# Kernel optimization log

Measured on AMD Instinct MI355X. Metric: run time of the kernel, lower is better.

The kernel has to match this reference:

```python
import jax, jax.numpy as jnp
import numpy as np

B, S, UNITS = 32, 2048, 512
D = 2 * UNITS  # 1024


def setup_inputs() -> dict:
    key = jax.random.key(0)
    ks = jax.random.split(key, 12)
    s = 1.0 / np.sqrt(D)
    mask = (jax.random.uniform(ks[0], (B, S)) < 0.9).astype(jnp.float32)
    mask = mask.at[:, 0].set(1.0)  # guarantee no all-zero row
    return {
        "dec_hidden": jax.random.normal(ks[1], (2, B, UNITS), dtype=jnp.float32),
        "enc_output": jax.random.normal(ks[2], (B, S, D), dtype=jnp.float32),
        "enc_pad_mask": mask,
        "prev_coverage": jax.random.uniform(ks[3], (B, S), dtype=jnp.float32) * 0.1,
        "Wh": jax.random.uniform(ks[4], (D, D), minval=-s, maxval=s),
        "bh": jax.random.uniform(ks[5], (D,), minval=-s, maxval=s),
        "Ws": jax.random.uniform(ks[6], (D, D), minval=-s, maxval=s),
        "bs": jax.random.uniform(ks[7], (D,), minval=-s, maxval=s),
        "Wc": jax.random.uniform(ks[8], (D, 1), minval=-1.0, maxval=1.0),
        "bc": jax.random.uniform(ks[9], (D,), minval=-1.0, maxval=1.0),
        "v": jax.random.uniform(ks[10], (1, D), minval=-s, maxval=s),
        "bv": jax.random.uniform(ks[11], (1,), minval=-s, maxval=s),
        "use_coverage": 1,
    }


def reference(dec_hidden, enc_output, enc_pad_mask, prev_coverage,
              Wh, bh, Ws, bs, Wc, bc, v, bv, use_coverage):
    # dec_hidden: (2, B, units) -> (B, 1, 2*units)
    dec = jnp.transpose(dec_hidden, (1, 0, 2)).reshape(dec_hidden.shape[1], 1, -1)
    enc_features = jnp.einsum('bsd,ed->bse', enc_output, Wh) + bh  # (B,S,D)
    dec_features = jnp.einsum('bod,ed->boe', dec, Ws) + bs          # (B,1,D)
    att_inputs = enc_features + dec_features
    if use_coverage:
        # Linear(1 -> D) applied to prev_coverage[..., None]
        coverage_features = prev_coverage[:, :, None] * Wc[:, 0][None, None, :] + bc
        att_inputs = att_inputs + coverage_features
    score = jnp.einsum('bsd,od->bso', jnp.tanh(att_inputs), v) + bv  # (B,S,1)
    attention_weights = jax.nn.softmax(score, axis=1)[..., 0]        # (B,S)
    attention_weights = attention_weights * enc_pad_mask
    attention_weights = attention_weights / jnp.sum(attention_weights, axis=1, keepdims=True)
    context_vector = jnp.einsum('bs,bsd->bd', attention_weights, enc_output)
    if use_coverage:
        coverage_vector = prev_coverage + attention_weights
        return context_vector, attention_weights, coverage_vector
    return context_vector, attention_weights
```

## Files before the change

### kernel.cpp

```cpp
#include <hip/hip_runtime.h>
#include <hip/hip_bf16.h>

#define BATCH 32
#define SEQ   2048
#define DIM   1024

typedef __attribute__((ext_vector_type(4))) float f32x4;
typedef __attribute__((ext_vector_type(8))) short short8;

static __device__ __forceinline__ ushort f2bf(float x) {
    __hip_bfloat16 h = __float2bfloat16(x);
    union { __hip_bfloat16 h; ushort u; } cv; cv.h = h;
    return cv.u;
}

__global__ __launch_bounds__(256) void kWhPack(const float* __restrict__ Wh,
                                               ushort* __restrict__ whbp) {
    int g = blockIdx.x * 256 + threadIdx.x;
    int l  = g & 63;
    int kb = (g >> 6) & 31;
    int eb = g >> 11;
    int e  = eb * 16 + (l & 15);
    int k0 = kb * 32 + (l >> 4) * 8;
    const float* src = Wh + (size_t)e * DIM + k0;
    float4 a = *(const float4*)src;
    float4 b = *(const float4*)(src + 4);
    union { ushort us[8]; uint4 u4; } pk;
    pk.us[0] = f2bf(a.x); pk.us[1] = f2bf(a.y); pk.us[2] = f2bf(a.z); pk.us[3] = f2bf(a.w);
    pk.us[4] = f2bf(b.x); pk.us[5] = f2bf(b.y); pk.us[6] = f2bf(b.z); pk.us[7] = f2bf(b.w);
    *(uint4*)(whbp + (size_t)g * 8) = pk.u4;
}

__global__ __launch_bounds__(256) void kBase(const float* __restrict__ dh,
                                             const float* __restrict__ Ws,
                                             const float* __restrict__ bs,
                                             const float* __restrict__ bh,
                                             const float* __restrict__ bc,
                                             const int* __restrict__ uc,
                                             float* __restrict__ base) {
    __shared__ float dec[8][DIM];
    int ec = blockIdx.x >> 2;
    int bg = blockIdx.x & 3;
    int b0 = bg * 8, e0 = ec * 32;
    int tid = threadIdx.x;
    for (int i = tid; i < 8 * DIM; i += 256) {
        int bb = i >> 10, d = i & 1023;
        float vdec = (d < 512) ? dh[(b0 + bb) * 512 + d]
                               : dh[BATCH * 512 + (b0 + bb) * 512 + d - 512];
        dec[bb][d] = vdec;
    }
    __syncthreads();
    int el = tid >> 3, ds = tid & 7;
    int e = e0 + el;
    float acc[8] = {0.f, 0.f, 0.f, 0.f, 0.f, 0.f, 0.f, 0.f};
    const float* wrow = Ws + (size_t)e * DIM;
    for (int i = 0; i < 128; ++i) {
        int d = i * 8 + ds;
        float wv = wrow[d];
#pragma unroll
        for (int bb = 0; bb < 8; ++bb) acc[bb] += wv * dec[bb][d];
    }
#pragma unroll
    for (int bb = 0; bb < 8; ++bb) {
        float s = acc[bb];
        s += __shfl_xor(s, 1); s += __shfl_xor(s, 2); s += __shfl_xor(s, 4);
        acc[bb] = s;
    }
    if (ds == 0) {
        float bias = bs[e] + bh[e] + ((*uc) ? bc[e] : 0.0f);
#pragma unroll
        for (int bb = 0; bb < 8; ++bb) base[(b0 + bb) * DIM + e] = acc[bb] + bias;
    }
}

__global__ __launch_bounds__(256, 4) void kScore(const float* __restrict__ enc,
                                                 const ushort* __restrict__ whbp,
                                                 const float* __restrict__ base,
                                                 const float* __restrict__ pc,
                                                 const float* __restrict__ Wc,
                                                 const float* __restrict__ vv,
                                                 const int* __restrict__ uc,
                                                 float* __restrict__ scorep) {
    __shared__ ushort Al[2][64 * 72];
    __shared__ float pcl[64];
    __shared__ float red[4][64];

    const int tid = threadIdx.x;
    const int w = tid >> 6;
    const int lane = tid & 63;
    const int q = lane >> 4, l15 = lane & 15;

    const int c = blockIdx.x & 7;
    const int j = blockIdx.x >> 3;
    const int strip = c * 128 + (j >> 2);
    const int nq = j & 3;
    const int b = strip >> 5;
    const int s0 = (strip & 31) << 6;

    const float* Ab = enc + ((size_t)(b * SEQ + s0)) * DIM;
    if (tid < 64) pcl[tid] = pc[b * SEQ + s0 + tid];

    const int r = tid & 63, kc = tid >> 6;
    const float* agp = Ab + (size_t)r * DIM + (kc << 4);
    const int awoff = r * 72 + (kc << 4);

    const ushort* bgp = whbp + ((size_t)((nq << 4) + (w << 2)) << 14) + (lane << 3);

    f32x4 acc[4][4] = {};

    {
        float4 v0 = *(const float4*)agp;
        float4 v1 = *(const float4*)(agp + 4);
        float4 v2 = *(const float4*)(agp + 8);
        float4 v3 = *(const float4*)(agp + 12);
        union { ushort us[8]; uint4 u4; } p0, p1;
        p0.us[0] = f2bf(v0.x); p0.us[1] = f2bf(v0.y); p0.us[2] = f2bf(v0.z); p0.us[3] = f2bf(v0.w);
        p0.us[4] = f2bf(v1.x); p0.us[5] = f2bf(v1.y); p0.us[6] = f2bf(v1.z); p0.us[7] = f2bf(v1.w);
        p1.us[0] = f2bf(v2.x); p1.us[1] = f2bf(v2.y); p1.us[2] = f2bf(v2.z); p1.us[3] = f2bf(v2.w);
        p1.us[4] = f2bf(v3.x); p1.us[5] = f2bf(v3.y); p1.us[6] = f2bf(v3.z); p1.us[7] = f2bf(v3.w);
        *(uint4*)&Al[0][awoff] = p0.u4;
        *(uint4*)&Al[0][awoff + 8] = p1.u4;
    }
    __syncthreads();

    int buf = 0;
    for (int kt = 0; kt < 16; ++kt) {
        float4 v0, v1, v2, v3;
        if (kt < 15) {
            const float* p = agp + (kt + 1) * 64;
            v0 = *(const float4*)p;       v1 = *(const float4*)(p + 4);
            v2 = *(const float4*)(p + 8); v3 = *(const float4*)(p + 12);
        }
#pragma unroll
        for (int kb = 0; kb < 2; ++kb) {
            short8 bf[4], af[4];
#pragma unroll
            for (int ef = 0; ef < 4; ++ef)
                bf[ef] = *(const short8*)(bgp + ((size_t)ef << 14) + ((size_t)((kt << 1) + kb) << 9));
#pragma unroll
            for (int mf = 0; mf < 4; ++mf)
                af[mf] = *(const short8*)&Al[buf][((mf << 4) + l15) * 72 + (kb << 5) + (q << 3)];
#pragma unroll
            for (int ef = 0; ef < 4; ++ef)
#pragma unroll
                for (int mf = 0; mf < 4; ++mf)
                    acc[mf][ef] = __builtin_amdgcn_mfma_f32_16x16x32_bf16(af[mf], bf[ef], acc[mf][ef], 0, 0, 0);
        }
        if (kt < 15) {
            union { ushort us[8]; uint4 u4; } p0, p1;
            p0.us[0] = f2bf(v0.x); p0.us[1] = f2bf(v0.y); p0.us[2] = f2bf(v0.z); p0.us[3] = f2bf(v0.w);
            p0.us[4] = f2bf(v1.x); p0.us[5] = f2bf(v1.y); p0.us[6] = f2bf(v1.z); p0.us[7] = f2bf(v1.w);
            p1.us[0] = f2bf(v2.x); p1.us[1] = f2bf(v2.y); p1.us[2] = f2bf(v2.z); p1.us[3] = f2bf(v2.w);
            p1.us[4] = f2bf(v3.x); p1.us[5] = f2bf(v3.y); p1.us[6] = f2bf(v3.z); p1.us[7] = f2bf(v3.w);
            *(uint4*)&Al[buf ^ 1][awoff] = p0.u4;
            *(uint4*)&Al[buf ^ 1][awoff + 8] = p1.u4;
        }
        __syncthreads();
        buf ^= 1;
    }

    const float ucf = (float)(*uc);
    float basee[4], ve[4], wce[4];
#pragma unroll
    for (int ef = 0; ef < 4; ++ef) {
        int e = (nq << 8) + (w << 6) + (ef << 4) + l15;
        basee[ef] = base[b * DIM + e];
        ve[ef] = vv[e];
        wce[ef] = Wc[e] * ucf;
    }
#pragma unroll
    for (int mf = 0; mf < 4; ++mf) {
#pragma unroll
        for (int rr = 0; rr < 4; ++rr) {
            int rl = (mf << 4) + (q << 2) + rr;
            float p = pcl[rl];
            float sp = 0.f;
#pragma unroll
            for (int ef = 0; ef < 4; ++ef) {
                float x = acc[mf][ef][rr] + basee[ef] + p * wce[ef];
                float t = 1.0f - 2.0f / (1.0f + __expf(2.0f * x));
                sp += t * ve[ef];
            }
            sp += __shfl_xor(sp, 1);
            sp += __shfl_xor(sp, 2);
            sp += __shfl_xor(sp, 4);
            sp += __shfl_xor(sp, 8);
            if (l15 == 0) red[w][rl] = sp;
        }
    }
    __syncthreads();
    if (tid < 64) {
        float s = red[0][tid] + red[1][tid] + red[2][tid] + red[3][tid];
        scorep[nq * (BATCH * SEQ) + b * SEQ + s0 + tid] = s;
    }
}

__global__ __launch_bounds__(512) void kSoftmax(const float* __restrict__ scorep,
                                                const float* __restrict__ mask,
                                                const float* __restrict__ pc,
                                                float* __restrict__ att,
                                                float* __restrict__ cov,
                                                int write_cov) {
    __shared__ float rmax[8], rsum[8];
    const int BS = BATCH * SEQ;
    int b = blockIdx.x, tid = threadIdx.x;
    int wv = tid >> 6, ln = tid & 63;
    float x[4];
#pragma unroll
    for (int i = 0; i < 4; ++i) {
        int idx = b * SEQ + tid + i * 512;
        x[i] = (scorep[idx] + scorep[BS + idx]) + (scorep[2 * BS + idx] + scorep[3 * BS + idx]);
    }
    float m = fmaxf(fmaxf(x[0], x[1]), fmaxf(x[2], x[3]));
#pragma unroll
    for (int o = 1; o < 64; o <<= 1) m = fmaxf(m, __shfl_xor(m, o));
    if (ln == 0) rmax[wv] = m;
    __syncthreads();
    m = rmax[0];
#pragma unroll
    for (int i = 1; i < 8; ++i) m = fmaxf(m, rmax[i]);

    float ms[4], wm[4];
#pragma unroll
    for (int i = 0; i < 4; ++i) ms[i] = mask[b * SEQ + tid + i * 512];
    float s = 0.f;
#pragma unroll
    for (int i = 0; i < 4; ++i) { wm[i] = __expf(x[i] - m) * ms[i]; s += wm[i]; }
#pragma unroll
    for (int o = 1; o < 64; o <<= 1) s += __shfl_xor(s, o);
    if (ln == 0) rsum[wv] = s;
    __syncthreads();
    s = 0.f;
#pragma unroll
    for (int i = 0; i < 8; ++i) s += rsum[i];
    float inv = 1.0f / s;
#pragma unroll
    for (int i = 0; i < 4; ++i) {
        float wf = wm[i] * inv;
        att[b * SEQ + tid + i * 512] = wf;
        if (write_cov) cov[b * SEQ + tid + i * 512] = pc[b * SEQ + tid + i * 512] + wf;
    }
}

__global__ __launch_bounds__(256) void kCtxPart(const float* __restrict__ enc,
                                                const float* __restrict__ att,
                                                float* __restrict__ part) {
    __shared__ float wl[64];
    int bx = blockIdx.x;
    int b = bx >> 5, sc = bx & 31;
    int tid = threadIdx.x;
    if (tid < 64) wl[tid] = att[b * SEQ + sc * 64 + tid];
    __syncthreads();
    const float* basep = enc + ((size_t)(b * SEQ + sc * 64)) * DIM + tid * 4;
    float4 acc = {0.f, 0.f, 0.f, 0.f};
#pragma unroll 4
    for (int i = 0; i < 64; ++i) {
        float w = wl[i];
        float4 xv = *(const float4*)(basep + (size_t)i * DIM);
        acc.x += w * xv.x; acc.y += w * xv.y; acc.z += w * xv.z; acc.w += w * xv.w;
    }
    *(float4*)(part + (size_t)bx * DIM + tid * 4) = acc;
}

__global__ __launch_bounds__(256) void kCtxReduce(const float* __restrict__ part,
                                                  float* __restrict__ ctx) {
    int g = blockIdx.x * 256 + threadIdx.x;
    int b = g >> 10, d = g & 1023;
    float s = 0.f;
#pragma unroll
    for (int i = 0; i < 32; ++i) s += part[((size_t)(b * 32 + i) << 10) + d];
    ctx[g] = s;
}

extern "C" void kernel_launch(void* const* d_in, const int* in_sizes, int n_in,
                              void* d_out, int out_size, void* d_ws, size_t ws_size,
                              hipStream_t stream) {
    const float* dh   = (const float*)d_in[0];
    const float* enc  = (const float*)d_in[1];
    const float* mask = (const float*)d_in[2];
    const float* pc   = (const float*)d_in[3];
    const float* Wh   = (const float*)d_in[4];
    const float* bh   = (const float*)d_in[5];
    const float* Ws   = (const float*)d_in[6];
    const float* bs   = (const float*)d_in[7];
    const float* Wc   = (const float*)d_in[8];
    const float* bc   = (const float*)d_in[9];
    const float* vv   = (const float*)d_in[10];
    const int* uc     = (const int*)d_in[12];

    float* ctx = (float*)d_out;
    float* att = ctx + BATCH * DIM;
    float* cov = att + BATCH * SEQ;
    int write_cov = (out_size >= BATCH * (DIM + 2 * SEQ)) ? 1 : 0;

    ushort* whbp  = (ushort*)d_ws;
    float* base   = (float*)((char*)d_ws + 2u * 1024u * 1024u);
    float* scorep = base + BATCH * DIM;
    float* part   = scorep + 4 * BATCH * SEQ;

    kWhPack<<<512, 256, 0, stream>>>(Wh, whbp);
    kBase<<<128, 256, 0, stream>>>(dh, Ws, bs, bh, bc, uc, base);
    kScore<<<4096, 256, 0, stream>>>(enc, whbp, base, pc, Wc, vv, uc, scorep);
    kSoftmax<<<BATCH, 512, 0, stream>>>(scorep, mask, pc, att, cov, write_cov);
    kCtxPart<<<1024, 256, 0, stream>>>(enc, att, part);
    kCtxReduce<<<128, 256, 0, stream>>>(part, ctx);
}
```

Measured before the change: 298.7 us.

## Enlarge kScore tile to 256x256 with async LDS loads for Wh

The score GEMM moves from a 64-row by 256-column tile per 256-thread block to a 256x256 tile per 512-thread block. Each wave now computes 128x64 outputs. Wh tiles are staged into LDS with global_load_lds direct loads, and enc rows are prefetched two k-steps ahead. Explicit waitcnt/barrier scheduling and s_setprio around the MFMA phases try to overlap loads with compute. The larger tile raises reuse of enc and Wh per block, cutting global and L2 traffic. The cost is much more LDS (about 128KB) and register pressure, and the grid drops to 1024 blocks.

```diff
diff --git a/kernel.cpp b/kernel.cpp
--- a/kernel.cpp
+++ b/kernel.cpp
@@ -12,6 +12,12 @@
     __hip_bfloat16 h = __float2bfloat16(x);
     union { __hip_bfloat16 h; ushort u; } cv; cv.h = h;
     return cv.u;
+}
+
+static __device__ __forceinline__ void gll16(const void* g, void* l) {
+    __builtin_amdgcn_global_load_lds(
+        (const __attribute__((address_space(1))) void*)g,
+        (__attribute__((address_space(3))) void*)l, 16, 0, 0);
 }
 
 __global__ __launch_bounds__(256) void kWhPack(const float* __restrict__ Wh,
@@ -73,7 +79,7 @@
     }
 }
 
-__global__ __launch_bounds__(256, 4) void kScore(const float* __restrict__ enc,
+__global__ __launch_bounds__(512, 2) void kScore(const float* __restrict__ enc,
                                                  const ushort* __restrict__ whbp,
                                                  const float* __restrict__ base,
                                                  const float* __restrict__ pc,
@@ -81,117 +87,146 @@
                                                  const float* __restrict__ vv,
                                                  const int* __restrict__ uc,
                                                  float* __restrict__ scorep) {
-    __shared__ ushort Al[2][64 * 72];
-    __shared__ float pcl[64];
-    __shared__ float red[4][64];
+    __shared__ ushort Al[2][16384];
+    __shared__ ushort Bl[2][16384];
+    __shared__ float pcl[256];
+    __shared__ float red[4][256];
 
     const int tid = threadIdx.x;
-    const int w = tid >> 6;
-    const int lane = tid & 63;
+    const int w = tid >> 6, lane = tid & 63;
     const int q = lane >> 4, l15 = lane & 15;
-
-    const int c = blockIdx.x & 7;
+    const int wm = w >> 2, wn = w & 3;
+
+    const int x = blockIdx.x & 7;
     const int j = blockIdx.x >> 3;
-    const int strip = c * 128 + (j >> 2);
-    const int nq = j & 3;
-    const int b = strip >> 5;
-    const int s0 = (strip & 31) << 6;
+    const int ms = x * 32 + (j >> 2);
+    const int nb = j & 3;
+    const int b = ms >> 3;
+    const int s0 = (ms & 7) << 8;
 
     const float* Ab = enc + ((size_t)(b * SEQ + s0)) * DIM;
-    if (tid < 64) pcl[tid] = pc[b * SEQ + s0 + tid];
-
-    const int r = tid & 63, kc = tid >> 6;
-    const float* agp = Ab + (size_t)r * DIM + (kc << 4);
-    const int awoff = r * 72 + (kc << 4);
-
-    const ushort* bgp = whbp + ((size_t)((nq << 4) + (w << 2)) << 14) + (lane << 3);
-
-    f32x4 acc[4][4] = {};
-
-    {
-        float4 v0 = *(const float4*)agp;
-        float4 v1 = *(const float4*)(agp + 4);
-        float4 v2 = *(const float4*)(agp + 8);
-        float4 v3 = *(const float4*)(agp + 12);
-        union { ushort us[8]; uint4 u4; } p0, p1;
-        p0.us[0] = f2bf(v0.x); p0.us[1] = f2bf(v0.y); p0.us[2] = f2bf(v0.z); p0.us[3] = f2bf(v0.w);
-        p0.us[4] = f2bf(v1.x); p0.us[5] = f2bf(v1.y); p0.us[6] = f2bf(v1.z); p0.us[7] = f2bf(v1.w);
-        p1.us[0] = f2bf(v2.x); p1.us[1] = f2bf(v2.y); p1.us[2] = f2bf(v2.z); p1.us[3] = f2bf(v2.w);
-        p1.us[4] = f2bf(v3.x); p1.us[5] = f2bf(v3.y); p1.us[6] = f2bf(v3.z); p1.us[7] = f2bf(v3.w);
-        *(uint4*)&Al[0][awoff] = p0.u4;
-        *(uint4*)&Al[0][awoff + 8] = p1.u4;
-    }
-    __syncthreads();
-
-    int buf = 0;
+    if (tid < 256) pcl[tid] = pc[b * SEQ + s0 + tid];
+
+    const float* agp[4];
+    int adst[4];
+#pragma unroll
+    for (int i = 0; i < 4; ++i) {
+        int fA = i * 8 + w, mt = fA >> 1, kb = fA & 1;
+        int row = mt * 16 + l15, kk = kb * 32 + q * 8;
+        agp[i] = Ab + (size_t)row * DIM + kk;
+        adst[i] = fA * 512 + lane * 8;
+    }
+    const ushort* bsrc[4];
+    int bdst[4];
+#pragma unroll
+    for (int c = 0; c < 4; ++c) {
+        int fB = c * 8 + w, ebl = fB >> 1, kbit = fB & 1;
+        bsrc[c] = whbp + ((size_t)((nb * 16 + ebl) * 32 + kbit)) * 512 + lane * 8;
+        bdst[c] = fB * 512;
+    }
+
+    f32x4 acc[8][4] = {};
+    float4 rA[8];
+
+#define CVT_WRITE(BUF) do { \
+    _Pragma("unroll") \
+    for (int i = 0; i < 4; ++i) { \
+        union { ushort us[8]; uint4 u4; } pk_; \
+        float4 lo = rA[2*i], hi = rA[2*i+1]; \
+        pk_.us[0]=f2bf(lo.x); pk_.us[1]=f2bf(lo.y); pk_.us[2]=f2bf(lo.z); pk_.us[3]=f2bf(lo.w); \
+        pk_.us[4]=f2bf(hi.x); pk_.us[5]=f2bf(hi.y); pk_.us[6]=f2bf(hi.z); pk_.us[7]=f2bf(hi.w); \
+        *(uint4*)&Al[BUF][adst[i]] = pk_.u4; \
+    } } while (0)
+
+#define ALOAD(KT) do { \
+    _Pragma("unroll") \
+    for (int i = 0; i < 4; ++i) { \
+        const float* p_ = agp[i] + (KT) * 64; \
+        rA[2*i] = *(const float4*)p_; rA[2*i+1] = *(const float4*)(p_ + 4); \
+    } } while (0)
+
+#define GLLB(KT, BUF) do { \
+    _Pragma("unroll") \
+    for (int c = 0; c < 4; ++c) \
+        gll16(bsrc[c] + (size_t)(KT) * 1024, &Bl[BUF][bdst[c]]); \
+    } while (0)
+
+#define MFMA_PHASE(BUF, KB) do { \
+    short8 a_[8], b_[4]; \
+    _Pragma("unroll") \
+    for (int mf = 0; mf < 8; ++mf) \
+        a_[mf] = *(const short8*)&Al[BUF][(((wm<<3)+mf)*2+(KB))*512 + (lane<<3)]; \
+    _Pragma("unroll") \
+    for (int ef = 0; ef < 4; ++ef) \
+        b_[ef] = *(const short8*)&Bl[BUF][(((wn<<2)+ef)*2+(KB))*512 + (lane<<3)]; \
+    __builtin_amdgcn_s_setprio(1); \
+    _Pragma("unroll") \
+    for (int ef = 0; ef < 4; ++ef) \
+        _Pragma("unroll") \
+        for (int mf = 0; mf < 8; ++mf) \
+            acc[mf][ef] = __builtin_amdgcn_mfma_f32_16x16x32_bf16(a_[mf], b_[ef], acc[mf][ef], 0, 0, 0); \
+    __builtin_amdgcn_s_setprio(0); \
+    } while (0)
+
+    ALOAD(0);
+    GLLB(0, 0);
+    CVT_WRITE(0);
+    ALOAD(1);
+    __syncthreads();
+    GLLB(1, 1);
+
     for (int kt = 0; kt < 16; ++kt) {
-        float4 v0, v1, v2, v3;
+        const int cur = kt & 1, nxt = cur ^ 1;
+        MFMA_PHASE(cur, 0);
         if (kt < 15) {
-            const float* p = agp + (kt + 1) * 64;
-            v0 = *(const float4*)p;       v1 = *(const float4*)(p + 4);
-            v2 = *(const float4*)(p + 8); v3 = *(const float4*)(p + 12);
+            CVT_WRITE(nxt);
+            if (kt < 14) ALOAD(kt + 2);
         }
-#pragma unroll
-        for (int kb = 0; kb < 2; ++kb) {
-            short8 bf[4], af[4];
-#pragma unroll
-            for (int ef = 0; ef < 4; ++ef)
-                bf[ef] = *(const short8*)(bgp + ((size_t)ef << 14) + ((size_t)((kt << 1) + kb) << 9));
-#pragma unroll
-            for (int mf = 0; mf < 4; ++mf)
-                af[mf] = *(const short8*)&Al[buf][((mf << 4) + l15) * 72 + (kb << 5) + (q << 3)];
-#pragma unroll
-            for (int ef = 0; ef < 4; ++ef)
-#pragma unroll
-                for (int mf = 0; mf < 4; ++mf)
-                    acc[mf][ef] = __builtin_amdgcn_mfma_f32_16x16x32_bf16(af[mf], bf[ef], acc[mf][ef], 0, 0, 0);
+        MFMA_PHASE(cur, 1);
+        if (kt < 15) {
+            asm volatile("s_waitcnt lgkmcnt(0)" ::: "memory");
+            if (kt < 14) { asm volatile("s_waitcnt vmcnt(8)" ::: "memory"); }
+            else         { asm volatile("s_waitcnt vmcnt(0)" ::: "memory"); }
+            __builtin_amdgcn_sched_barrier(0);
+            __builtin_amdgcn_s_barrier();
+            __builtin_amdgcn_sched_barrier(0);
+            if (kt < 14) GLLB(kt + 2, cur);
         }
-        if (kt < 15) {
-            union { ushort us[8]; uint4 u4; } p0, p1;
-            p0.us[0] = f2bf(v0.x); p0.us[1] = f2bf(v0.y); p0.us[2] = f2bf(v0.z); p0.us[3] = f2bf(v0.w);
-            p0.us[4] = f2bf(v1.x); p0.us[5] = f2bf(v1.y); p0.us[6] = f2bf(v1.z); p0.us[7] = f2bf(v1.w);
-            p1.us[0] = f2bf(v2.x); p1.us[1] = f2bf(v2.y); p1.us[2] = f2bf(v2.z); p1.us[3] = f2bf(v2.w);
-            p1.us[4] = f2bf(v3.x); p1.us[5] = f2bf(v3.y); p1.us[6] = f2bf(v3.z); p1.us[7] = f2bf(v3.w);
-            *(uint4*)&Al[buf ^ 1][awoff] = p0.u4;
-            *(uint4*)&Al[buf ^ 1][awoff + 8] = p1.u4;
-        }
-        __syncthreads();
-        buf ^= 1;
     }
 
     const float ucf = (float)(*uc);
     float basee[4], ve[4], wce[4];
 #pragma unroll
     for (int ef = 0; ef < 4; ++ef) {
-        int e = (nq << 8) + (w << 6) + (ef << 4) + l15;
+        int e = (nb << 8) + ((wn << 2) + ef) * 16 + l15;
         basee[ef] = base[b * DIM + e];
         ve[ef] = vv[e];
         wce[ef] = Wc[e] * ucf;
     }
 #pragma unroll
-    for (int mf = 0; mf < 4; ++mf) {
-#pragma unroll
-        for (int rr = 0; rr < 4; ++rr) {
-            int rl = (mf << 4) + (q << 2) + rr;
+    for (int mf = 0; mf < 8; ++mf) {
+#pragma unroll
+        for (int r = 0; r < 4; ++r) {
+            int rl = (wm << 7) + (mf << 4) + (q << 2) + r;
             float p = pcl[rl];
             float sp = 0.f;
 #pragma unroll
             for (int ef = 0; ef < 4; ++ef) {
-                float x = acc[mf][ef][rr] + basee[ef] + p * wce[ef];
-                float t = 1.0f - 2.0f / (1.0f + __expf(2.0f * x));
+                float xv = acc[mf][ef][r] + basee[ef] + p * wce[ef];
+                float t = 1.0f - 2.0f / (1.0f + __expf(2.0f * xv));
                 sp += t * ve[ef];
             }
             sp += __shfl_xor(sp, 1);
             sp += __shfl_xor(sp, 2);
             sp += __shfl_xor(sp, 4);
             sp += __shfl_xor(sp, 8);
-            if (l15 == 0) red[w][rl] = sp;
+            if (l15 == 0) red[wn][rl] = sp;
         }
     }
     __syncthreads();
-    if (tid < 64) {
-        float s = red[0][tid] + red[1][tid] + red[2][tid] + red[3][tid];
-        scorep[nq * (BATCH * SEQ) + b * SEQ + s0 + tid] = s;
+    if (tid < 256) {
+        float s = (red[0][tid] + red[1][tid]) + (red[2][tid] + red[3][tid]);
+        scorep[nb * (BATCH * SEQ) + b * SEQ + s0 + tid] = s;
     }
 }
 
@@ -300,7 +335,7 @@
 
     kWhPack<<<512, 256, 0, stream>>>(Wh, whbp);
     kBase<<<128, 256, 0, stream>>>(dh, Ws, bs, bh, bc, uc, base);
-    kScore<<<4096, 256, 0, stream>>>(enc, whbp, base, pc, Wc, vv, uc, scorep);
+    kScore<<<1024, 512, 0, stream>>>(enc, whbp, base, pc, Wc, vv, uc, scorep);
     kSoftmax<<<BATCH, 512, 0, stream>>>(scorep, mask, pc, att, cov, write_cov);
     kCtxPart<<<1024, 256, 0, stream>>>(enc, att, part);
     kCtxReduce<<<128, 256, 0, stream>>>(part, ctx);
```

Measured after the change: 289.9 us. 1.03x faster.
